# Performance work log

Measured on AMD Instinct MI355X. Metric: run time of the kernel, lower is better.

The kernel has to match this reference:

```python
import jax, jax.numpy as jnp
import numpy as np

B, HR, WR, C = 64, 64, 64, 256
NH, WS, SS = 8, 8, 4
HD = C // NH
N = WS * WS
NW = (HR // WS) * (WR // WS)
CRPB_H = 384
MLP_H = 4 * C
EPS = 1e-5


def _rel_tables():
    r = np.arange(-(WS - 1), WS, dtype=np.float32)
    tbl = np.stack(np.meshgrid(r, r, indexing='ij'), axis=-1)[None]  # (1,2W-1,2W-1,2)
    tbl = tbl / (WS - 1)
    tbl = tbl * 8.0
    tbl = np.sign(tbl) * np.log2(np.abs(tbl) + 1.0) / np.log2(8.0)
    ch, cw = np.meshgrid(np.arange(WS), np.arange(WS), indexing='ij')
    coords = np.stack([ch.ravel(), cw.ravel()])            # (2, N)
    rel = (coords[:, :, None] - coords[:, None, :]).transpose(1, 2, 0)
    rel[:, :, 0] += WS - 1
    rel[:, :, 1] += WS - 1
    rel[:, :, 0] *= 2 * WS - 1
    idx = rel.sum(-1)                                      # (N, N)
    return jnp.asarray(tbl, jnp.float32), jnp.asarray(idx, jnp.int32)


def _attn_mask():
    img = np.zeros((HR, WR), np.float32)
    cnt = 0
    sl = [slice(0, -WS), slice(-WS, -SS), slice(-SS, None)]
    for h in sl:
        for w in sl:
            img[h, w] = cnt
            cnt += 1
    mw = img.reshape(HR // WS, WS, WR // WS, WS).transpose(0, 2, 1, 3).reshape(-1, N)
    diff = mw[:, None, :] - mw[:, :, None]
    return jnp.asarray(np.where(diff != 0, -100.0, 0.0).astype(np.float32))


_REL_TBL, _REL_IDX = _rel_tables()
_MASK = _attn_mask()


def _ln(x, w, b):
    m = jnp.mean(x, axis=-1, keepdims=True)
    v = jnp.mean((x - m) ** 2, axis=-1, keepdims=True)
    return (x - m) / jnp.sqrt(v + EPS) * w + b


def setup_inputs() -> dict:
    key = jax.random.key(0)
    ks = jax.random.split(key, 20)
    s = 0.02
    return {
        'x': jax.random.normal(ks[0], (B, HR * WR, C), jnp.float32),
        'qkv_w': jax.random.normal(ks[1], (3 * C, C), jnp.float32) * s,
        'qkv_b': jnp.zeros((3 * C,), jnp.float32),
        'proj_w': jax.random.normal(ks[2], (C, C), jnp.float32) * s,
        'proj_b': jnp.zeros((C,), jnp.float32),
        't_scale': jnp.log(10.0 * jnp.ones((NH, 1, 1), jnp.float32)),
        'crpb_w1': jax.random.normal(ks[3], (CRPB_H, 2), jnp.float32) * s,
        'crpb_b1': jnp.zeros((CRPB_H,), jnp.float32),
        'crpb_w2': jax.random.normal(ks[4], (NH, CRPB_H), jnp.float32) * s,
        'norm1_w': jnp.ones((C,), jnp.float32),
        'norm1_b': jnp.zeros((C,), jnp.float32),
        'norm2_w': jnp.ones((C,), jnp.float32),
        'norm2_b': jnp.zeros((C,), jnp.float32),
        'fc1_w': jax.random.normal(ks[5], (MLP_H, C), jnp.float32) * s,
        'fc1_b': jnp.zeros((MLP_H,), jnp.float32),
        'fc2_w': jax.random.normal(ks[6], (C, MLP_H), jnp.float32) * s,
        'fc2_b': jnp.zeros((C,), jnp.float32),
    }


def reference(x, qkv_w, qkv_b, proj_w, proj_b, t_scale, crpb_w1, crpb_b1,
              crpb_w2, norm1_w, norm1_b, norm2_w, norm2_b,
              fc1_w, fc1_b, fc2_w, fc2_b):
    shortcut = x
    xi = x.reshape(B, HR, WR, C)
    # cyclic shift
    xi = jnp.roll(xi, shift=(-SS, -SS), axis=(1, 2))
    # window partition -> (B*nW, N, C)
    xw = xi.reshape(B, HR // WS, WS, WR // WS, WS, C)
    xw = xw.transpose(0, 1, 3, 2, 4, 5).reshape(-1, N, C)
    Bw = xw.shape[0]

    # qkv
    qkv = xw @ qkv_w.T + qkv_b                       # (Bw, N, 3C)
    qkv = qkv.reshape(Bw, N, 3, NH, HD).transpose(2, 0, 3, 1, 4)
    q, k, v = qkv[0], qkv[1], qkv[2]                 # (Bw, NH, N, HD)

    # cosine attention with clamped learned temperature
    qn = q / jnp.clip(jnp.linalg.norm(q, axis=-1, keepdims=True), 1e-12)
    kn = k / jnp.clip(jnp.linalg.norm(k, axis=-1, keepdims=True), 1e-12)
    scale = jnp.exp(jnp.minimum(t_scale, jnp.log(1.0 / 0.01)))  # (NH,1,1)
    attn = jnp.einsum('bhnd,bhmd->bhnm', qn, kn) * scale

    # continuous relative position bias via MLP + gather
    h = jax.nn.relu(_REL_TBL @ crpb_w1.T + crpb_b1)            # (1,2W-1,2W-1,384)
    table = (h @ crpb_w2.T).reshape(-1, NH)                    # ((2W-1)^2, NH)
    bias = table[_REL_IDX.reshape(-1)].reshape(N, N, NH).transpose(2, 0, 1)
    bias = 16.0 * jax.nn.sigmoid(bias)
    attn = attn + bias[None]

    # shifted-window mask
    attn = attn.reshape(B, NW, NH, N, N) + _MASK[None, :, None]
    attn = jax.nn.softmax(attn.reshape(Bw, NH, N, N), axis=-1)

    out = jnp.einsum('bhnm,bhmd->bhnd', attn, v)
    out = out.transpose(0, 2, 1, 3).reshape(Bw, N, C)
    out = out @ proj_w.T + proj_b

    # window reverse + reverse shift
    out = out.reshape(B, HR // WS, WR // WS, WS, WS, C)
    out = out.transpose(0, 1, 3, 2, 4, 5).reshape(B, HR, WR, C)
    out = jnp.roll(out, shift=(SS, SS), axis=(1, 2)).reshape(B, HR * WR, C)

    # Swin-V2 post-norm residuals
    xo = shortcut + _ln(out, norm1_w, norm1_b)
    m = jax.nn.gelu(xo @ fc1_w.T + fc1_b, approximate=False)
    m = m @ fc2_w.T + fc2_b
    return xo + _ln(m, norm2_w, norm2_b)
```

## Files before the change

### kernel.cpp

```cpp
#include <hip/hip_runtime.h>

typedef float f32x4 __attribute__((ext_vector_type(4)));
typedef _Float16 f16;
typedef _Float16 f16x8 __attribute__((ext_vector_type(8)));
typedef unsigned int u32;
typedef unsigned short u16;

__device__ __forceinline__ u16 f2h(float f){
  f16 h = (f16)f; return __builtin_bit_cast(u16, h);
}
__device__ __forceinline__ float h2f(u16 u){
  f16 h = __builtin_bit_cast(f16, u); return (float)h;
}
__device__ __forceinline__ f16x8 ld16(const void* p){
  uint4 v = *(const uint4*)p;
  return __builtin_bit_cast(f16x8, v);
}
__device__ __forceinline__ f32x4 mm(f16x8 a, f16x8 b, f32x4 c){
  return __builtin_amdgcn_mfma_f32_16x16x32_f16(a, b, c, 0, 0, 0);
}

__global__ void k_wconv(const float* __restrict__ qkvw, const float* __restrict__ projw,
                        const float* __restrict__ fc1w, const float* __restrict__ fc2w,
                        u16* __restrict__ o_qkv, u16* __restrict__ o_proj,
                        u16* __restrict__ o_fc1, u16* __restrict__ o_fc2){
  int t = blockIdx.x*256 + threadIdx.x;
  int frag = t >> 6, lane = t & 63;
  int l15 = lane & 15, g = lane >> 4;
  const float* src; u16* dst; int col, k, ld, f;
  if(frag < 384){
    f = frag;
    int part = f >> 7, rem = f & 127;
    int h = rem >> 4, rem2 = rem & 15;
    int tc = rem2 >> 3, kk = rem2 & 7;
    col = part*256 + h*32 + tc*16 + l15; k = kk*32 + g*8;
    src = qkvw; dst = o_qkv; ld = 256;
  } else if(frag < 512){
    f = frag - 384;
    int w = f >> 4, rem = f & 15;
    int tn = rem >> 3, kk = rem & 7;
    col = w*32 + tn*16 + l15; k = kk*32 + g*8;
    src = projw; dst = o_proj; ld = 256;
  } else if(frag < 1024){
    f = frag - 512;
    int ck = f >> 6, rem = f & 63;
    int wn = rem >> 4, rem2 = rem & 15;
    int tn = rem2 >> 3, kk = rem2 & 7;
    col = ck*128 + wn*32 + tn*16 + l15; k = kk*32 + g*8;
    src = fc1w; dst = o_fc1; ld = 256;
  } else {
    f = frag - 1024;
    int wn = f >> 7, rem = f & 127;
    int tn = rem >> 5, rem2 = rem & 31;
    int ck = rem2 >> 2, kk2 = rem2 & 3;
    col = wn*64 + tn*16 + l15; k = ck*128 + kk2*32 + g*8;
    src = fc2w; dst = o_fc2; ld = 1024;
  }
  float4 a = *(const float4*)(src + (size_t)col*ld + k);
  float4 b4 = *(const float4*)(src + (size_t)col*ld + k + 4);
  ushort4 h0, h1;
  h0.x=f2h(a.x); h0.y=f2h(a.y); h0.z=f2h(a.z); h0.w=f2h(a.w);
  h1.x=f2h(b4.x); h1.y=f2h(b4.y); h1.z=f2h(b4.z); h1.w=f2h(b4.w);
  u16* o = dst + (size_t)f*512 + lane*8;
  *(ushort4*)o = h0;
  *(ushort4*)(o+4) = h1;
}

__global__ void k_bias(const float* __restrict__ w1, const float* __restrict__ b1,
                       const float* __restrict__ w2, float* __restrict__ bias){
  __shared__ float tab[225][8];
  int t = threadIdx.x;
  if(t < 225){
    int i15 = t/15, j15 = t%15;
    float di = (float)(i15-7) * (8.f/7.f);
    float dj = (float)(j15-7) * (8.f/7.f);
    float vi = copysignf(log2f(fabsf(di)+1.f)*(1.f/3.f), di);
    float vj = copysignf(log2f(fabsf(dj)+1.f)*(1.f/3.f), dj);
    float acc[8];
    #pragma unroll
    for(int h=0;h<8;h++) acc[h]=0.f;
    for(int c=0;c<384;c++){
      float hv = vi*w1[c*2] + vj*w1[c*2+1] + b1[c];
      hv = fmaxf(hv, 0.f);
      #pragma unroll
      for(int h=0;h<8;h++) acc[h] += hv * w2[h*384+c];
    }
    #pragma unroll
    for(int h=0;h<8;h++) tab[t][h] = acc[h];
  }
  __syncthreads();
  for(int pr = t; pr < 4096; pr += 256){
    int i = pr>>6, j = pr&63;
    int dh = (i>>3)-(j>>3)+7, dw = (i&7)-(j&7)+7;
    int idx = dh*15+dw;
    #pragma unroll
    for(int h=0;h<8;h++){
      float v = tab[idx][h];
      bias[(h*64+i)*64+j] = 16.f / (1.f + __expf(-v));
    }
  }
}

__global__ __launch_bounds__(512, 1)
void k_attn(const float* __restrict__ x, const u16* __restrict__ qkvw,
            const float* __restrict__ qkvb, const u16* __restrict__ projw,
            const float* __restrict__ projb, const float* __restrict__ tsc,
            const float* __restrict__ biastab,
            const float* __restrict__ n1w, const float* __restrict__ n1b,
            u16* __restrict__ y)
{
  extern __shared__ char sm[];
  const int tid = threadIdx.x;
  const int w = tid >> 6, lane = tid & 63;
  const int l15 = lane & 15, g = lane >> 4;
  const int blk = blockIdx.x;
  const int b = blk >> 6, nw = blk & 63, wh = nw >> 3, wwi = nw & 7;

  char* Wq = sm + 32768 + w*12288;
  char* Wk = Wq + 4096;
  char* Wv = Wq + 8192;
  char* Wp = Wq;
  float* nrmq = (float*)(sm + 131072 + w*512);
  float* nrmk = nrmq + 64;

  {
    int row = tid >> 3, seg = tid & 7;
    int hs = ((wh<<3) + (row>>3) + 4) & 63;
    int ws_ = ((wwi<<3) + (row&7) + 4) & 63;
    const float* src = x + (size_t)(b*4096 + hs*64 + ws_)*256 + seg*32;
    char* drow = sm + row*512;
    int sw = (row & 7) << 4;
    #pragma unroll
    for(int u=0; u<4; u++){
      float4 f0 = ((const float4*)src)[2*u];
      float4 f1 = ((const float4*)src)[2*u+1];
      uint4 pk;
      pk.x = (u32)f2h(f0.x) | ((u32)f2h(f0.y)<<16);
      pk.y = (u32)f2h(f0.z) | ((u32)f2h(f0.w)<<16);
      pk.z = (u32)f2h(f1.x) | ((u32)f2h(f1.y)<<16);
      pk.w = (u32)f2h(f1.z) | ((u32)f2h(f1.w)<<16);
      *(uint4*)(drow + (((seg<<6) + (u<<4)) ^ sw)) = pk;
    }
  }
  __syncthreads();

  const int h = w;
  #pragma unroll
  for(int part=0; part<3; part++){
    f32x4 acc[2][4] = {};
    #pragma unroll
    for(int kk=0; kk<8; kk++){
      f16x8 a[4];
      #pragma unroll
      for(int tm=0; tm<4; tm++){
        int row = tm*16 + l15;
        a[tm] = ld16(sm + row*512 + (((kk<<6) + (g<<4)) ^ ((row&7)<<4)));
      }
      #pragma unroll
      for(int tc=0; tc<2; tc++){
        f16x8 bf = ld16(qkvw + (size_t)(part*128 + h*16 + tc*8 + kk)*512 + lane*8);
        #pragma unroll
        for(int tm=0; tm<4; tm++) acc[tc][tm] = mm(a[tm], bf, acc[tc][tm]);
      }
    }
    #pragma unroll
    for(int tc=0; tc<2; tc++){
      float bv = qkvb[part*256 + h*32 + tc*16 + l15];
      #pragma unroll
      for(int tm=0; tm<4; tm++){
        #pragma unroll
        for(int r=0; r<4; r++){
          float val = acc[tc][tm][r] + bv;
          int tok = tm*16 + g*4 + r;
          int col = tc*16 + l15;
          u16 hv = f2h(val);
          if(part==0)      *(u16*)(Wq + (tok<<6) + ((col<<1) ^ ((tok&3)<<4))) = hv;
          else if(part==1) *(u16*)(Wk + (tok<<6) + ((col<<1) ^ ((tok&3)<<4))) = hv;
          else             *(u16*)(Wv + (col<<7) + ((tok<<1) ^ ((col&7)<<4))) = hv;
        }
      }
    }
  }

  {
    float sq = 0.f, sk = 0.f;
    #pragma unroll
    for(int cb=0; cb<4; cb++){
      f16x8 qv = ld16(Wq + (lane<<6) + ((cb<<4) ^ ((lane&3)<<4)));
      f16x8 kv = ld16(Wk + (lane<<6) + ((cb<<4) ^ ((lane&3)<<4)));
      #pragma unroll
      for(int j=0;j<8;j++){ float a=(float)qv[j]; sq+=a*a; float c=(float)kv[j]; sk+=c*c; }
    }
    float sc = __expf(fminf(tsc[h], 4.605170185988091f));
    nrmq[lane] = sc / fmaxf(sqrtf(sq), 1e-12f);
    nrmk[lane] = 1.f / fmaxf(sqrtf(sk), 1e-12f);
  }
  __syncthreads();

  f32x4 s[4][4];
  float rsum[4][4];
  {
    f16x8 qf[4], kf[4];
    #pragma unroll
    for(int tm=0; tm<4; tm++){
      int row = tm*16 + l15;
      qf[tm] = ld16(Wq + (row<<6) + ((g<<4) ^ ((row&3)<<4)));
      kf[tm] = ld16(Wk + (row<<6) + ((g<<4) ^ ((row&3)<<4)));
    }
    const f32x4 z4 = {0.f,0.f,0.f,0.f};
    #pragma unroll
    for(int tm=0; tm<4; tm++)
      #pragma unroll
      for(int tn=0; tn<4; tn++)
        s[tm][tn] = mm(qf[tm], kf[tn], z4);
  }
  {
    int idj[4]; float nk[4];
    #pragma unroll
    for(int tn=0; tn<4; tn++){
      int j = tn*16 + l15;
      nk[tn] = nrmk[j];
      int hsj = (wh<<3) + (j>>3), wsj = (wwi<<3) + (j&7);
      idj[tn] = 3*((hsj<56)?0:((hsj<60)?1:2)) + ((wsj<56)?0:((wsj<60)?1:2));
    }
    #pragma unroll
    for(int tm=0; tm<4; tm++){
      #pragma unroll
      for(int r=0; r<4; r++){
        int i = tm*16 + g*4 + r;
        float nq = nrmq[i];
        int hsi = (wh<<3) + (i>>3), wsi = (wwi<<3) + (i&7);
        int idi = 3*((hsi<56)?0:((hsi<60)?1:2)) + ((wsi<56)?0:((wsi<60)?1:2));
        float vr[4];
        #pragma unroll
        for(int tn=0; tn<4; tn++){
          int j = tn*16 + l15;
          float bv = biastab[((h<<6)+i)*64 + j];
          vr[tn] = s[tm][tn][r]*nq*nk[tn] + bv + ((idi!=idj[tn]) ? -100.f : 0.f);
        }
        float mx = fmaxf(fmaxf(vr[0],vr[1]), fmaxf(vr[2],vr[3]));
        mx = fmaxf(mx, __shfl_xor(mx, 1));
        mx = fmaxf(mx, __shfl_xor(mx, 2));
        mx = fmaxf(mx, __shfl_xor(mx, 4));
        mx = fmaxf(mx, __shfl_xor(mx, 8));
        float sumv = 0.f;
        #pragma unroll
        for(int tn=0; tn<4; tn++){
          float p = exp2f((vr[tn]-mx)*1.4426950408889634f);
          sumv += p;
          vr[tn] = p;
        }
        sumv += __shfl_xor(sumv, 1);
        sumv += __shfl_xor(sumv, 2);
        sumv += __shfl_xor(sumv, 4);
        sumv += __shfl_xor(sumv, 8);
        rsum[tm][r] = sumv;
        #pragma unroll
        for(int tn=0; tn<4; tn++){
          int j = tn*16 + l15;
          *(u16*)(Wp + (i<<7) + ((j<<1) ^ ((i&7)<<4))) = f2h(vr[tn]);
        }
      }
    }
  }
  f32x4 o[4][2] = {};
  #pragma unroll
  for(int kk=0; kk<2; kk++){
    f16x8 pf[4];
    #pragma unroll
    for(int tm=0; tm<4; tm++){
      int row = tm*16 + l15;
      pf[tm] = ld16(Wp + (row<<7) + (((kk<<6)+(g<<4)) ^ ((row&7)<<4)));
    }
    #pragma unroll
    for(int tn=0; tn<2; tn++){
      int n = tn*16 + l15;
      f16x8 vf = ld16(Wv + (n<<7) + (((kk<<6)+(g<<4)) ^ ((n&7)<<4)));
      #pragma unroll
      for(int tm=0; tm<4; tm++) o[tm][tn] = mm(pf[tm], vf, o[tm][tn]);
    }
  }
  #pragma unroll
  for(int tm=0; tm<4; tm++)
    #pragma unroll
    for(int tn=0; tn<2; tn++)
      #pragma unroll
      for(int r=0; r<4; r++){
        int i = tm*16 + g*4 + r;
        int col = h*32 + tn*16 + l15;
        float val = o[tm][tn][r] / rsum[tm][r];
        *(u16*)(sm + (i<<9) + ((col<<1) ^ ((i&7)<<4))) = f2h(val);
      }
  __syncthreads();

  {
    float* yr32 = (float*)(sm + 32768);
    f32x4 pa[4][2] = {};
    #pragma unroll
    for(int kk=0; kk<8; kk++){
      f16x8 a[4];
      #pragma unroll
      for(int tm=0; tm<4; tm++){
        int row = tm*16 + l15;
        a[tm] = ld16(sm + (row<<9) + (((kk<<6)+(g<<4)) ^ ((row&7)<<4)));
      }
      #pragma unroll
      for(int tn=0; tn<2; tn++){
        f16x8 bf = ld16(projw + (size_t)(w*16 + tn*8 + kk)*512 + lane*8);
        #pragma unroll
        for(int tm=0; tm<4; tm++) pa[tm][tn] = mm(a[tm], bf, pa[tm][tn]);
      }
    }
    #pragma unroll
    for(int tn=0; tn<2; tn++){
      float pb = projb[w*32 + tn*16 + l15];
      #pragma unroll
      for(int tm=0; tm<4; tm++)
        #pragma unroll
        for(int r=0; r<4; r++){
          int tok = tm*16 + g*4 + r;
          int col = w*32 + tn*16 + l15;
          yr32[tok*256 + (col ^ ((tok&7)<<2))] = pa[tm][tn][r] + pb;
        }
    }
  }
  __syncthreads();

  {
    int row = tid >> 3, seg = tid & 7;
    const float* yr = (const float*)(sm + 32768) + row*256;
    int sw4 = (row&7)<<2;
    float yv[32];
    float s1 = 0.f, s2 = 0.f;
    #pragma unroll
    for(int t=0; t<8; t++){
      float4 v4 = *(const float4*)(yr + ((seg*32 + t*4) ^ sw4));
      yv[t*4+0]=v4.x; yv[t*4+1]=v4.y; yv[t*4+2]=v4.z; yv[t*4+3]=v4.w;
      s1 += v4.x+v4.y+v4.z+v4.w;
      s2 += v4.x*v4.x+v4.y*v4.y+v4.z*v4.z+v4.w*v4.w;
    }
    s1 += __shfl_xor(s1,1); s2 += __shfl_xor(s2,1);
    s1 += __shfl_xor(s1,2); s2 += __shfl_xor(s2,2);
    s1 += __shfl_xor(s1,4); s2 += __shfl_xor(s2,4);
    float mean = s1*(1.f/256.f);
    float var = s2*(1.f/256.f) - mean*mean;
    float rstd = rsqrtf(var + 1e-5f);
    u32 hw[16];
    #pragma unroll
    for(int j=0; j<32; j++){
      int c = seg*32 + j;
      float zz = (yv[j]-mean)*rstd*n1w[c] + n1b[c];
      u16 hv = f2h(zz);
      if(j&1) hw[j>>1] |= ((u32)hv)<<16; else hw[j>>1] = (u32)hv;
    }
    int ho = ((wh<<3) + (row>>3) + 4) & 63;
    int wo = ((wwi<<3) + (row&7) + 4) & 63;
    u16* dst = y + (size_t)(b*4096 + ho*64 + wo)*256 + seg*32;
    #pragma unroll
    for(int u2=0; u2<4; u2++)
      ((uint4*)dst)[u2] = *(uint4*)(&hw[u2*4]);
  }
}

__global__ __attribute__((amdgpu_waves_per_eu(4,4))) __launch_bounds__(256)
void k_mlp(const float* __restrict__ x, const u16* __restrict__ z,
           const u16* __restrict__ fc1, const float* __restrict__ f1b,
           const u16* __restrict__ fc2, const float* __restrict__ f2bb,
           const float* __restrict__ n2w, const float* __restrict__ n2b,
           float* __restrict__ out)
{
  __shared__ char smem[24576];
  char* xo16 = smem;
  char* hbf  = smem + 16384;
  const int tid = threadIdx.x;
  const int wn = tid>>6, lane = tid&63, l15 = lane&15, g = lane>>4;
  const size_t row0 = (size_t)blockIdx.x * 32;

  {
    int row = tid>>3, seg = tid&7;
    size_t grow = row0 + row;
    const u16* zp = z + grow*256 + seg*32;
    const float* xp = x + grow*256 + seg*32;
    int swb = (row&7)<<4;
    #pragma unroll
    for(int u=0;u<4;u++){
      uint4 raw = ((const uint4*)zp)[u];
      float4 xa = ((const float4*)xp)[2*u];
      float4 xb = ((const float4*)xp)[2*u+1];
      u32 rw[4] = {raw.x, raw.y, raw.z, raw.w};
      float v[8];
      v[0] = xa.x + h2f((u16)(rw[0] & 0xFFFFu));
      v[1] = xa.y + h2f((u16)(rw[0] >> 16));
      v[2] = xa.z + h2f((u16)(rw[1] & 0xFFFFu));
      v[3] = xa.w + h2f((u16)(rw[1] >> 16));
      v[4] = xb.x + h2f((u16)(rw[2] & 0xFFFFu));
      v[5] = xb.y + h2f((u16)(rw[2] >> 16));
      v[6] = xb.z + h2f((u16)(rw[3] & 0xFFFFu));
      v[7] = xb.w + h2f((u16)(rw[3] >> 16));
      u32 pw[4];
      #pragma unroll
      for(int j=0;j<8;j++){
        if(j&1) pw[j>>1] |= ((u32)f2h(v[j]))<<16; else pw[j>>1] = (u32)f2h(v[j]);
      }
      uint4 pk; pk.x=pw[0]; pk.y=pw[1]; pk.z=pw[2]; pk.w=pw[3];
      *(uint4*)(xo16 + (row<<9) + (((seg<<6)+(u<<4)) ^ swb)) = pk;
    }
  }
  __syncthreads();

  f32x4 acc2[2][4] = {};
  for(int ck=0; ck<8; ck++){
    f32x4 a1[2][2] = {{{0.f,0.f,0.f,0.f},{0.f,0.f,0.f,0.f}},
                      {{0.f,0.f,0.f,0.f},{0.f,0.f,0.f,0.f}}};
    {
      const u16* fb = fc1 + ((size_t)(ck*64 + wn*16))*512 + (size_t)lane*8;
      f16x8 bc0 = ld16(fb);
      f16x8 bc1 = ld16(fb + 8*512);
      #pragma unroll
      for(int kk=0; kk<8; kk++){
        f16x8 nb0, nb1;
        if(kk < 7){
          nb0 = ld16(fb + (size_t)(kk+1)*512);
          nb1 = ld16(fb + (size_t)(8+kk+1)*512);
        }
        f16x8 af0, af1;
        {
          int row = l15;
          af0 = ld16(xo16 + (row<<9) + (((kk<<6)+(g<<4)) ^ ((row&7)<<4)));
          row = 16 + l15;
          af1 = ld16(xo16 + (row<<9) + (((kk<<6)+(g<<4)) ^ ((row&7)<<4)));
        }
        a1[0][0] = mm(af0, bc0, a1[0][0]);
        a1[1][0] = mm(af1, bc0, a1[1][0]);
        a1[0][1] = mm(af0, bc1, a1[0][1]);
        a1[1][1] = mm(af1, bc1, a1[1][1]);
        bc0 = nb0; bc1 = nb1;
      }
    }
    #pragma unroll
    for(int tn=0;tn<2;tn++){
      float bv = f1b[ck*128 + wn*32 + tn*16 + l15];
      #pragma unroll
      for(int tm=0;tm<2;tm++)
        #pragma unroll
        for(int r=0;r<4;r++){
          float zv = a1[tm][tn][r] + bv;
          float u0 = 0.7978845608028654f*(zv + 0.044715f*zv*zv*zv);
          float e = exp2f(u0 * 2.8853900817779268f);
          float th = 1.f - 2.f/(e+1.f);
          float ge = 0.5f*zv*(1.f+th);
          int row = tm*16 + g*4 + r;
          int hc = wn*32 + tn*16 + l15;
          *(u16*)(hbf + (row<<8) + ((hc<<1) ^ ((row&7)<<4))) = f2h(ge);
        }
    }
    __syncthreads();
    {
      const u16* gb = fc2 + ((size_t)(wn*128 + ck*4))*512 + (size_t)lane*8;
      f16x8 c0 = ld16(gb);
      f16x8 c1 = ld16(gb + 32*512);
      f16x8 c2 = ld16(gb + 64*512);
      f16x8 c3 = ld16(gb + 96*512);
      #pragma unroll
      for(int kk2=0; kk2<4; kk2++){
        f16x8 n0,n1,n2,n3;
        if(kk2 < 3){
          n0 = ld16(gb + (size_t)(kk2+1)*512);
          n1 = ld16(gb + (size_t)(32+kk2+1)*512);
          n2 = ld16(gb + (size_t)(64+kk2+1)*512);
          n3 = ld16(gb + (size_t)(96+kk2+1)*512);
        }
        f16x8 af0, af1;
        {
          int row = l15;
          af0 = ld16(hbf + (row<<8) + (((kk2<<6)+(g<<4)) ^ ((row&7)<<4)));
          row = 16 + l15;
          af1 = ld16(hbf + (row<<8) + (((kk2<<6)+(g<<4)) ^ ((row&7)<<4)));
        }
        acc2[0][0] = mm(af0, c0, acc2[0][0]);
        acc2[1][0] = mm(af1, c0, acc2[1][0]);
        acc2[0][1] = mm(af0, c1, acc2[0][1]);
        acc2[1][1] = mm(af1, c1, acc2[1][1]);
        acc2[0][2] = mm(af0, c2, acc2[0][2]);
        acc2[1][2] = mm(af1, c2, acc2[1][2]);
        acc2[0][3] = mm(af0, c3, acc2[0][3]);
        acc2[1][3] = mm(af1, c3, acc2[1][3]);
        c0=n0; c1=n1; c2=n2; c3=n3;
      }
    }
    __syncthreads();
  }

  {
    float b2v[4], w2v[4], b2n[4];
    #pragma unroll
    for(int tn=0;tn<4;tn++){
      int col = wn*64 + tn*16 + l15;
      b2v[tn] = f2bb[col];
      w2v[tn] = n2w[col];
      b2n[tn] = n2b[col];
    }
    #pragma unroll
    for(int tm=0;tm<2;tm++)
      #pragma unroll
      for(int tn=0;tn<4;tn++)
        #pragma unroll
        for(int r=0;r<4;r++) acc2[tm][tn][r] += b2v[tn];

    float* lnp = (float*)hbf;
    #pragma unroll
    for(int tm=0;tm<2;tm++)
      #pragma unroll
      for(int r=0;r<4;r++){
        float sA=0.f, sB=0.f;
        #pragma unroll
        for(int tn=0;tn<4;tn++){ float v=acc2[tm][tn][r]; sA+=v; sB+=v*v; }
        sA += __shfl_xor(sA,1); sB += __shfl_xor(sB,1);
        sA += __shfl_xor(sA,2); sB += __shfl_xor(sB,2);
        sA += __shfl_xor(sA,4); sB += __shfl_xor(sB,4);
        sA += __shfl_xor(sA,8); sB += __shfl_xor(sB,8);
        if(l15==0){
          int row = tm*16 + g*4 + r;
          lnp[(row*4+wn)*2]   = sA;
          lnp[(row*4+wn)*2+1] = sB;
        }
      }
    __syncthreads();
    #pragma unroll
    for(int tm=0;tm<2;tm++)
      #pragma unroll
      for(int r=0;r<4;r++){
        int row = tm*16 + g*4 + r;
        float S=0.f, SS=0.f;
        #pragma unroll
        for(int q2=0;q2<4;q2++){ S += lnp[(row*4+q2)*2]; SS += lnp[(row*4+q2)*2+1]; }
        float mean = S*(1.f/256.f);
        float var = SS*(1.f/256.f) - mean*mean;
        float rstd = rsqrtf(var + 1e-5f);
        float* op = out + (row0 + row)*256;
        #pragma unroll
        for(int tn=0;tn<4;tn++){
          int col = wn*64 + tn*16 + l15;
          float xo = h2f(*(const u16*)(xo16 + (row<<9) + ((col<<1) ^ ((row&7)<<4))));
          op[col] = xo + (acc2[tm][tn][r]-mean)*rstd*w2v[tn] + b2n[tn];
        }
      }
  }
}

extern "C" void kernel_launch(void* const* d_in, const int* in_sizes, int n_in,
                              void* d_out, int out_size, void* d_ws, size_t ws_size,
                              hipStream_t stream)
{
  const float* x     = (const float*)d_in[0];
  const float* qkvw  = (const float*)d_in[1];
  const float* qkvb  = (const float*)d_in[2];
  const float* projw = (const float*)d_in[3];
  const float* projb = (const float*)d_in[4];
  const float* tsc   = (const float*)d_in[5];
  const float* w1    = (const float*)d_in[6];
  const float* b1    = (const float*)d_in[7];
  const float* w2    = (const float*)d_in[8];
  const float* n1w   = (const float*)d_in[9];
  const float* n1b   = (const float*)d_in[10];
  const float* n2w   = (const float*)d_in[11];
  const float* n2b   = (const float*)d_in[12];
  const float* fc1w  = (const float*)d_in[13];
  const float* fc1b  = (const float*)d_in[14];
  const float* fc2w  = (const float*)d_in[15];
  const float* fc2b  = (const float*)d_in[16];
  float* out = (float*)d_out;

  char* ws = (char*)d_ws;
  const size_t WB = 134217728;
  u16* z_h      = (u16*)(ws);
  u16* qkvw_h   = (u16*)(ws + WB);
  u16* projw_h  = (u16*)(ws + WB + 393216);
  u16* fc1_h    = (u16*)(ws + WB + 524288);
  u16* fc2_h    = (u16*)(ws + WB + 1048576);
  float* biastab= (float*)(ws + WB + 1572864);

  hipFuncSetAttribute((const void*)k_attn,
                      hipFuncAttributeMaxDynamicSharedMemorySize, 135168);

  k_wconv<<<384, 256, 0, stream>>>(qkvw, projw, fc1w, fc2w,
                                   qkvw_h, projw_h, fc1_h, fc2_h);
  k_bias<<<1, 256, 0, stream>>>(w1, b1, w2, biastab);
  k_attn<<<4096, 512, 135168, stream>>>(x, qkvw_h, qkvb, projw_h, projb,
                                        tsc, biastab, n1w, n1b, z_h);
  k_mlp<<<8192, 256, 0, stream>>>(x, z_h, fc1_h, fc1b,
                                  fc2_h, fc2b, n2w, n2b, out);
}
```

Before: 1.043 ms.

## Restructure window attention to 4 waves handling two heads each, halving LDS

The attention kernel now runs 256 threads per block, with each wave handling two heads one after the other. V fragments are built in registers through lane shuffles instead of being staged in shared memory, and the per-row norms are shared by shuffles rather than LDS. The projection output is kept in fp16 instead of fp32, and conversions use packed cvt_pkrtz. Together these cut dynamic LDS from 132KB to 64KB so two blocks can fit per CU. The cost is more serial work per wave, extra register pressure, and a round-to-zero conversion plus fp16 rounding of the projection output before LayerNorm, which slightly changes numerics.

```diff
diff --git a/kernel.cpp b/kernel.cpp
--- a/kernel.cpp
+++ b/kernel.cpp
@@ -11,6 +11,10 @@
 }
 __device__ __forceinline__ float h2f(u16 u){
   f16 h = __builtin_bit_cast(f16, u); return (float)h;
+}
+__device__ __forceinline__ u32 pkh2(float a, float b){
+  auto r = __builtin_amdgcn_cvt_pkrtz(a, b);
+  return __builtin_bit_cast(u32, r);
 }
 __device__ __forceinline__ f16x8 ld16(const void* p){
   uint4 v = *(const uint4*)p;
@@ -37,9 +41,9 @@
     src = qkvw; dst = o_qkv; ld = 256;
   } else if(frag < 512){
     f = frag - 384;
-    int w = f >> 4, rem = f & 15;
-    int tn = rem >> 3, kk = rem & 7;
-    col = w*32 + tn*16 + l15; k = kk*32 + g*8;
+    int w8 = f >> 4, rem = f & 15;
+    int tn2 = rem >> 3, kk = rem & 7;
+    col = w8*32 + tn2*16 + l15; k = kk*32 + g*8;
     src = projw; dst = o_proj; ld = 256;
   } else if(frag < 1024){
     f = frag - 512;
@@ -101,7 +105,7 @@
   }
 }
 
-__global__ __launch_bounds__(512, 1)
+__global__ __launch_bounds__(256, 2)
 void k_attn(const float* __restrict__ x, const u16* __restrict__ qkvw,
             const float* __restrict__ qkvb, const u16* __restrict__ projw,
             const float* __restrict__ projb, const float* __restrict__ tsc,
@@ -116,15 +120,13 @@
   const int blk = blockIdx.x;
   const int b = blk >> 6, nw = blk & 63, wh = nw >> 3, wwi = nw & 7;
 
-  char* Wq = sm + 32768 + w*12288;
+  char* Wq = sm + 32768 + w*8192;
   char* Wk = Wq + 4096;
-  char* Wv = Wq + 8192;
   char* Wp = Wq;
-  float* nrmq = (float*)(sm + 131072 + w*512);
-  float* nrmk = nrmq + 64;
-
-  {
-    int row = tid >> 3, seg = tid & 7;
+
+  #pragma unroll
+  for(int p=0; p<2; p++){
+    int row = (tid >> 3) + p*32, seg = tid & 7;
     int hs = ((wh<<3) + (row>>3) + 4) & 63;
     int ws_ = ((wwi<<3) + (row&7) + 4) & 63;
     const float* src = x + (size_t)(b*4096 + hs*64 + ws_)*256 + seg*32;
@@ -135,167 +137,218 @@
       float4 f0 = ((const float4*)src)[2*u];
       float4 f1 = ((const float4*)src)[2*u+1];
       uint4 pk;
-      pk.x = (u32)f2h(f0.x) | ((u32)f2h(f0.y)<<16);
-      pk.y = (u32)f2h(f0.z) | ((u32)f2h(f0.w)<<16);
-      pk.z = (u32)f2h(f1.x) | ((u32)f2h(f1.y)<<16);
-      pk.w = (u32)f2h(f1.z) | ((u32)f2h(f1.w)<<16);
+      pk.x = pkh2(f0.x, f0.y);
+      pk.y = pkh2(f0.z, f0.w);
+      pk.z = pkh2(f1.x, f1.y);
+      pk.w = pkh2(f1.z, f1.w);
       *(uint4*)(drow + (((seg<<6) + (u<<4)) ^ sw)) = pk;
     }
   }
   __syncthreads();
 
-  const int h = w;
+  f32x4 o0[4][2];
+  float rs0[4][4];
+
   #pragma unroll
-  for(int part=0; part<3; part++){
-    f32x4 acc[2][4] = {};
-    #pragma unroll
-    for(int kk=0; kk<8; kk++){
-      f16x8 a[4];
+  for(int hh=0; hh<2; hh++){
+    const int h = w*2 + hh;
+    f16x8 vfrag[2][2];
+
+    #pragma unroll
+    for(int part=0; part<3; part++){
+      f32x4 acc[2][4] = {};
+      #pragma unroll
+      for(int kk=0; kk<8; kk++){
+        f16x8 a[4];
+        #pragma unroll
+        for(int tm=0; tm<4; tm++){
+          int row = tm*16 + l15;
+          a[tm] = ld16(sm + row*512 + (((kk<<6) + (g<<4)) ^ ((row&7)<<4)));
+        }
+        #pragma unroll
+        for(int tc=0; tc<2; tc++){
+          f16x8 bf = ld16(qkvw + (size_t)(part*128 + h*16 + tc*8 + kk)*512 + lane*8);
+          #pragma unroll
+          for(int tm=0; tm<4; tm++) acc[tc][tm] = mm(a[tm], bf, acc[tc][tm]);
+        }
+      }
+      if(part < 2){
+        #pragma unroll
+        for(int tc=0; tc<2; tc++){
+          float bv = qkvb[part*256 + h*32 + tc*16 + l15];
+          char* Wqk = (part==0) ? Wq : Wk;
+          #pragma unroll
+          for(int tm=0; tm<4; tm++){
+            #pragma unroll
+            for(int r=0; r<4; r++){
+              int tok = tm*16 + g*4 + r;
+              int col = tc*16 + l15;
+              *(u16*)(Wqk + (tok<<6) + ((col<<1) ^ ((tok&3)<<4))) = f2h(acc[tc][tm][r] + bv);
+            }
+          }
+        }
+      } else {
+        u32 pk2[2][4][2];
+        #pragma unroll
+        for(int tc=0; tc<2; tc++){
+          float bv = qkvb[512 + h*32 + tc*16 + l15];
+          #pragma unroll
+          for(int tm=0; tm<4; tm++){
+            pk2[tc][tm][0] = pkh2(acc[tc][tm][0]+bv, acc[tc][tm][1]+bv);
+            pk2[tc][tm][1] = pkh2(acc[tc][tm][2]+bv, acc[tc][tm][3]+bv);
+          }
+        }
+        #pragma unroll
+        for(int kk=0; kk<2; kk++)
+          #pragma unroll
+          for(int tc=0; tc<2; tc++){
+            u32 d[4];
+            #pragma unroll
+            for(int u=0; u<4; u++){
+              int sl = l15 + ((((g&1)<<1) | (u>>1)) << 4);
+              u32 lo = (u32)__shfl((int)pk2[tc][kk*2  ][u&1], sl);
+              u32 hi = (u32)__shfl((int)pk2[tc][kk*2+1][u&1], sl);
+              d[u] = (g & 2) ? hi : lo;
+            }
+            uint4 q4; q4.x=d[0]; q4.y=d[1]; q4.z=d[2]; q4.w=d[3];
+            vfrag[kk][tc] = __builtin_bit_cast(f16x8, q4);
+          }
+      }
+    }
+
+    if(hh==1) __syncthreads();
+
+    float nrmq_r, nrmk_r;
+    {
+      float sq = 0.f, sk = 0.f;
+      #pragma unroll
+      for(int cb=0; cb<4; cb++){
+        f16x8 qv = ld16(Wq + (lane<<6) + ((cb<<4) ^ ((lane&3)<<4)));
+        f16x8 kv = ld16(Wk + (lane<<6) + ((cb<<4) ^ ((lane&3)<<4)));
+        #pragma unroll
+        for(int j=0;j<8;j++){ float a=(float)qv[j]; sq+=a*a; float c=(float)kv[j]; sk+=c*c; }
+      }
+      float sc = __expf(fminf(tsc[h], 4.605170185988091f));
+      nrmq_r = sc / fmaxf(sqrtf(sq), 1e-12f);
+      nrmk_r = 1.f / fmaxf(sqrtf(sk), 1e-12f);
+    }
+
+    f32x4 s[4][4];
+    float rsum[4][4];
+    {
+      f16x8 qf[4], kf[4];
       #pragma unroll
       for(int tm=0; tm<4; tm++){
         int row = tm*16 + l15;
-        a[tm] = ld16(sm + row*512 + (((kk<<6) + (g<<4)) ^ ((row&7)<<4)));
-      }
-      #pragma unroll
-      for(int tc=0; tc<2; tc++){
-        f16x8 bf = ld16(qkvw + (size_t)(part*128 + h*16 + tc*8 + kk)*512 + lane*8);
-        #pragma unroll
-        for(int tm=0; tm<4; tm++) acc[tc][tm] = mm(a[tm], bf, acc[tc][tm]);
-      }
-    }
-    #pragma unroll
-    for(int tc=0; tc<2; tc++){
-      float bv = qkvb[part*256 + h*32 + tc*16 + l15];
+        qf[tm] = ld16(Wq + (row<<6) + ((g<<4) ^ ((row&3)<<4)));
+        kf[tm] = ld16(Wk + (row<<6) + ((g<<4) ^ ((row&3)<<4)));
+      }
+      const f32x4 z4 = {0.f,0.f,0.f,0.f};
+      #pragma unroll
+      for(int tm=0; tm<4; tm++)
+        #pragma unroll
+        for(int tn=0; tn<4; tn++)
+          s[tm][tn] = mm(qf[tm], kf[tn], z4);
+    }
+    {
+      int idj[4]; float nk[4];
+      #pragma unroll
+      for(int tn=0; tn<4; tn++){
+        int j = tn*16 + l15;
+        nk[tn] = __shfl(nrmk_r, j);
+        int hsj = (wh<<3) + (j>>3), wsj = (wwi<<3) + (j&7);
+        idj[tn] = 3*((hsj<56)?0:((hsj<60)?1:2)) + ((wsj<56)?0:((wsj<60)?1:2));
+      }
       #pragma unroll
       for(int tm=0; tm<4; tm++){
         #pragma unroll
         for(int r=0; r<4; r++){
-          float val = acc[tc][tm][r] + bv;
-          int tok = tm*16 + g*4 + r;
-          int col = tc*16 + l15;
-          u16 hv = f2h(val);
-          if(part==0)      *(u16*)(Wq + (tok<<6) + ((col<<1) ^ ((tok&3)<<4))) = hv;
-          else if(part==1) *(u16*)(Wk + (tok<<6) + ((col<<1) ^ ((tok&3)<<4))) = hv;
-          else             *(u16*)(Wv + (col<<7) + ((tok<<1) ^ ((col&7)<<4))) = hv;
-        }
-      }
-    }
-  }
+          int i = tm*16 + g*4 + r;
+          float nq = __shfl(nrmq_r, i);
+          int hsi = (wh<<3) + (i>>3), wsi = (wwi<<3) + (i&7);
+          int idi = 3*((hsi<56)?0:((hsi<60)?1:2)) + ((wsi<56)?0:((wsi<60)?1:2));
+          float vr[4];
+          #pragma unroll
+          for(int tn=0; tn<4; tn++){
+            int j = tn*16 + l15;
+            float bv = biastab[((h<<6)+i)*64 + j];
+            vr[tn] = s[tm][tn][r]*nq*nk[tn] + bv + ((idi!=idj[tn]) ? -100.f : 0.f);
+          }
+          float mx = fmaxf(fmaxf(vr[0],vr[1]), fmaxf(vr[2],vr[3]));
+          mx = fmaxf(mx, __shfl_xor(mx, 1));
+          mx = fmaxf(mx, __shfl_xor(mx, 2));
+          mx = fmaxf(mx, __shfl_xor(mx, 4));
+          mx = fmaxf(mx, __shfl_xor(mx, 8));
+          float sumv = 0.f;
+          #pragma unroll
+          for(int tn=0; tn<4; tn++){
+            float pval = exp2f((vr[tn]-mx)*1.4426950408889634f);
+            sumv += pval;
+            vr[tn] = pval;
+          }
+          sumv += __shfl_xor(sumv, 1);
+          sumv += __shfl_xor(sumv, 2);
+          sumv += __shfl_xor(sumv, 4);
+          sumv += __shfl_xor(sumv, 8);
+          rsum[tm][r] = sumv;
+          #pragma unroll
+          for(int tn=0; tn<4; tn++){
+            int j = tn*16 + l15;
+            *(u16*)(Wp + (i<<7) + ((j<<1) ^ ((i&7)<<4))) = f2h(vr[tn]);
+          }
+        }
+      }
+    }
+    f32x4 o[4][2] = {};
+    #pragma unroll
+    for(int kk=0; kk<2; kk++){
+      f16x8 pf[4];
+      #pragma unroll
+      for(int tm=0; tm<4; tm++){
+        int row = tm*16 + l15;
+        pf[tm] = ld16(Wp + (row<<7) + (((kk<<6)+(g<<4)) ^ ((row&7)<<4)));
+      }
+      #pragma unroll
+      for(int tn=0; tn<2; tn++)
+        #pragma unroll
+        for(int tm=0; tm<4; tm++) o[tm][tn] = mm(pf[tm], vfrag[kk][tn], o[tm][tn]);
+    }
+    if(hh==0){
+      #pragma unroll
+      for(int tm=0; tm<4; tm++){
+        #pragma unroll
+        for(int tn=0; tn<2; tn++) o0[tm][tn] = o[tm][tn];
+        #pragma unroll
+        for(int r=0; r<4; r++) rs0[tm][r] = rsum[tm][r];
+      }
+    } else {
+      #pragma unroll
+      for(int tm=0; tm<4; tm++)
+        #pragma unroll
+        for(int tn=0; tn<2; tn++)
+          #pragma unroll
+          for(int r=0; r<4; r++){
+            int i = tm*16 + g*4 + r;
+            int col = h*32 + tn*16 + l15;
+            *(u16*)(sm + (i<<9) + ((col<<1) ^ ((i&7)<<4))) = f2h(o[tm][tn][r] / rsum[tm][r]);
+          }
+      #pragma unroll
+      for(int tm=0; tm<4; tm++)
+        #pragma unroll
+        for(int tn=0; tn<2; tn++)
+          #pragma unroll
+          for(int r=0; r<4; r++){
+            int i = tm*16 + g*4 + r;
+            int col = (w*2)*32 + tn*16 + l15;
+            *(u16*)(sm + (i<<9) + ((col<<1) ^ ((i&7)<<4))) = f2h(o0[tm][tn][r] / rs0[tm][r]);
+          }
+    }
+  }
+  __syncthreads();
 
   {
-    float sq = 0.f, sk = 0.f;
-    #pragma unroll
-    for(int cb=0; cb<4; cb++){
-      f16x8 qv = ld16(Wq + (lane<<6) + ((cb<<4) ^ ((lane&3)<<4)));
-      f16x8 kv = ld16(Wk + (lane<<6) + ((cb<<4) ^ ((lane&3)<<4)));
-      #pragma unroll
-      for(int j=0;j<8;j++){ float a=(float)qv[j]; sq+=a*a; float c=(float)kv[j]; sk+=c*c; }
-    }
-    float sc = __expf(fminf(tsc[h], 4.605170185988091f));
-    nrmq[lane] = sc / fmaxf(sqrtf(sq), 1e-12f);
-    nrmk[lane] = 1.f / fmaxf(sqrtf(sk), 1e-12f);
-  }
-  __syncthreads();
-
-  f32x4 s[4][4];
-  float rsum[4][4];
-  {
-    f16x8 qf[4], kf[4];
-    #pragma unroll
-    for(int tm=0; tm<4; tm++){
-      int row = tm*16 + l15;
-      qf[tm] = ld16(Wq + (row<<6) + ((g<<4) ^ ((row&3)<<4)));
-      kf[tm] = ld16(Wk + (row<<6) + ((g<<4) ^ ((row&3)<<4)));
-    }
-    const f32x4 z4 = {0.f,0.f,0.f,0.f};
-    #pragma unroll
-    for(int tm=0; tm<4; tm++)
-      #pragma unroll
-      for(int tn=0; tn<4; tn++)
-        s[tm][tn] = mm(qf[tm], kf[tn], z4);
-  }
-  {
-    int idj[4]; float nk[4];
-    #pragma unroll
-    for(int tn=0; tn<4; tn++){
-      int j = tn*16 + l15;
-      nk[tn] = nrmk[j];
-      int hsj = (wh<<3) + (j>>3), wsj = (wwi<<3) + (j&7);
-      idj[tn] = 3*((hsj<56)?0:((hsj<60)?1:2)) + ((wsj<56)?0:((wsj<60)?1:2));
-    }
-    #pragma unroll
-    for(int tm=0; tm<4; tm++){
-      #pragma unroll
-      for(int r=0; r<4; r++){
-        int i = tm*16 + g*4 + r;
-        float nq = nrmq[i];
-        int hsi = (wh<<3) + (i>>3), wsi = (wwi<<3) + (i&7);
-        int idi = 3*((hsi<56)?0:((hsi<60)?1:2)) + ((wsi<56)?0:((wsi<60)?1:2));
-        float vr[4];
-        #pragma unroll
-        for(int tn=0; tn<4; tn++){
-          int j = tn*16 + l15;
-          float bv = biastab[((h<<6)+i)*64 + j];
-          vr[tn] = s[tm][tn][r]*nq*nk[tn] + bv + ((idi!=idj[tn]) ? -100.f : 0.f);
-        }
-        float mx = fmaxf(fmaxf(vr[0],vr[1]), fmaxf(vr[2],vr[3]));
-        mx = fmaxf(mx, __shfl_xor(mx, 1));
-        mx = fmaxf(mx, __shfl_xor(mx, 2));
-        mx = fmaxf(mx, __shfl_xor(mx, 4));
-        mx = fmaxf(mx, __shfl_xor(mx, 8));
-        float sumv = 0.f;
-        #pragma unroll
-        for(int tn=0; tn<4; tn++){
-          float p = exp2f((vr[tn]-mx)*1.4426950408889634f);
-          sumv += p;
-          vr[tn] = p;
-        }
-        sumv += __shfl_xor(sumv, 1);
-        sumv += __shfl_xor(sumv, 2);
-        sumv += __shfl_xor(sumv, 4);
-        sumv += __shfl_xor(sumv, 8);
-        rsum[tm][r] = sumv;
-        #pragma unroll
-        for(int tn=0; tn<4; tn++){
-          int j = tn*16 + l15;
-          *(u16*)(Wp + (i<<7) + ((j<<1) ^ ((i&7)<<4))) = f2h(vr[tn]);
-        }
-      }
-    }
-  }
-  f32x4 o[4][2] = {};
-  #pragma unroll
-  for(int kk=0; kk<2; kk++){
-    f16x8 pf[4];
-    #pragma unroll
-    for(int tm=0; tm<4; tm++){
-      int row = tm*16 + l15;
-      pf[tm] = ld16(Wp + (row<<7) + (((kk<<6)+(g<<4)) ^ ((row&7)<<4)));
-    }
-    #pragma unroll
-    for(int tn=0; tn<2; tn++){
-      int n = tn*16 + l15;
-      f16x8 vf = ld16(Wv + (n<<7) + (((kk<<6)+(g<<4)) ^ ((n&7)<<4)));
-      #pragma unroll
-      for(int tm=0; tm<4; tm++) o[tm][tn] = mm(pf[tm], vf, o[tm][tn]);
-    }
-  }
-  #pragma unroll
-  for(int tm=0; tm<4; tm++)
-    #pragma unroll
-    for(int tn=0; tn<2; tn++)
-      #pragma unroll
-      for(int r=0; r<4; r++){
-        int i = tm*16 + g*4 + r;
-        int col = h*32 + tn*16 + l15;
-        float val = o[tm][tn][r] / rsum[tm][r];
-        *(u16*)(sm + (i<<9) + ((col<<1) ^ ((i&7)<<4))) = f2h(val);
-      }
-  __syncthreads();
-
-  {
-    float* yr32 = (float*)(sm + 32768);
-    f32x4 pa[4][2] = {};
+    char* yr16 = sm + 32768;
+    f32x4 pa[4][4] = {};
     #pragma unroll
     for(int kk=0; kk<8; kk++){
       f16x8 a[4];
@@ -305,39 +358,46 @@
         a[tm] = ld16(sm + (row<<9) + (((kk<<6)+(g<<4)) ^ ((row&7)<<4)));
       }
       #pragma unroll
-      for(int tn=0; tn<2; tn++){
-        f16x8 bf = ld16(projw + (size_t)(w*16 + tn*8 + kk)*512 + lane*8);
+      for(int tn=0; tn<4; tn++){
+        int fragi = (w*2 + (tn>>1))*16 + (tn&1)*8 + kk;
+        f16x8 bf = ld16(projw + (size_t)fragi*512 + lane*8);
         #pragma unroll
         for(int tm=0; tm<4; tm++) pa[tm][tn] = mm(a[tm], bf, pa[tm][tn]);
       }
     }
     #pragma unroll
-    for(int tn=0; tn<2; tn++){
-      float pb = projb[w*32 + tn*16 + l15];
+    for(int tn=0; tn<4; tn++){
+      float pb = projb[w*64 + tn*16 + l15];
       #pragma unroll
       for(int tm=0; tm<4; tm++)
         #pragma unroll
         for(int r=0; r<4; r++){
           int tok = tm*16 + g*4 + r;
-          int col = w*32 + tn*16 + l15;
-          yr32[tok*256 + (col ^ ((tok&7)<<2))] = pa[tm][tn][r] + pb;
+          int col = w*64 + tn*16 + l15;
+          *(u16*)(yr16 + (tok<<9) + ((col<<1) ^ ((tok&7)<<4))) = f2h(pa[tm][tn][r] + pb);
         }
     }
   }
   __syncthreads();
 
-  {
-    int row = tid >> 3, seg = tid & 7;
-    const float* yr = (const float*)(sm + 32768) + row*256;
-    int sw4 = (row&7)<<2;
+  #pragma unroll
+  for(int p=0; p<2; p++){
+    int row = (tid >> 3) + p*32, seg = tid & 7;
+    const char* yr = sm + 32768 + (row<<9);
+    int swb = (row&7)<<4;
     float yv[32];
     float s1 = 0.f, s2 = 0.f;
     #pragma unroll
-    for(int t=0; t<8; t++){
-      float4 v4 = *(const float4*)(yr + ((seg*32 + t*4) ^ sw4));
-      yv[t*4+0]=v4.x; yv[t*4+1]=v4.y; yv[t*4+2]=v4.z; yv[t*4+3]=v4.w;
-      s1 += v4.x+v4.y+v4.z+v4.w;
-      s2 += v4.x*v4.x+v4.y*v4.y+v4.z*v4.z+v4.w*v4.w;
+    for(int u=0; u<4; u++){
+      uint4 raw = *(const uint4*)(yr + (((seg<<6)+(u<<4)) ^ swb));
+      u32 rw[4] = {raw.x, raw.y, raw.z, raw.w};
+      #pragma unroll
+      for(int q2=0; q2<4; q2++){
+        float v0 = h2f((u16)(rw[q2] & 0xFFFFu));
+        float v1 = h2f((u16)(rw[q2] >> 16));
+        yv[u*8+q2*2] = v0; yv[u*8+q2*2+1] = v1;
+        s1 += v0+v1; s2 += v0*v0+v1*v1;
+      }
     }
     s1 += __shfl_xor(s1,1); s2 += __shfl_xor(s2,1);
     s1 += __shfl_xor(s1,2); s2 += __shfl_xor(s2,2);
@@ -580,14 +640,14 @@
   u16* fc2_h    = (u16*)(ws + WB + 1048576);
   float* biastab= (float*)(ws + WB + 1572864);
 
-  hipFuncSetAttribute((const void*)k_attn,
-                      hipFuncAttributeMaxDynamicSharedMemorySize, 135168);
+  (void)hipFuncSetAttribute((const void*)k_attn,
+                      hipFuncAttributeMaxDynamicSharedMemorySize, 65536);
 
   k_wconv<<<384, 256, 0, stream>>>(qkvw, projw, fc1w, fc2w,
                                    qkvw_h, projw_h, fc1_h, fc2_h);
   k_bias<<<1, 256, 0, stream>>>(w1, b1, w2, biastab);
-  k_attn<<<4096, 512, 135168, stream>>>(x, qkvw_h, qkvb, projw_h, projb,
-                                        tsc, biastab, n1w, n1b, z_h);
+  k_attn<<<4096, 256, 65536, stream>>>(x, qkvw_h, qkvb, projw_h, projb,
+                                       tsc, biastab, n1w, n1b, z_h);
   k_mlp<<<8192, 256, 0, stream>>>(x, z_h, fc1_h, fc1b,
                                   fc2_h, fc2b, n2w, n2b, out);
 }
```

New measurement: 1.275 ms. +22.3%, slower.
